# Kernel optimization log

Hardware: AMD Instinct MI355X
Metric: run time of the kernel (lower is better)

## Reference

```python
import jax, jax.numpy as jnp
import numpy as np

L, D, F, H = 4, 1024, 2048, 8
DH = D // H
EPS = 1e-5


def setup_inputs() -> dict:
    key = jax.random.key(0)
    ks = jax.random.split(key, 8)
    B, S = 4, 1024
    sd = 1.0 / np.sqrt(D)
    sf = 1.0 / np.sqrt(F)
    return {
        "X": jax.random.normal(ks[0], (B, S, D), jnp.float32),
        "Wq": jax.random.normal(ks[1], (L, D, D), jnp.float32) * sd,
        "Wk": jax.random.normal(ks[2], (L, D, D), jnp.float32) * sd,
        "Wv": jax.random.normal(ks[3], (L, D, D), jnp.float32) * sd,
        "Wg": jax.random.normal(ks[4], (L, D, D), jnp.float32) * sd,
        "Wo": jax.random.normal(ks[5], (L, D, D), jnp.float32) * sd,
        "W1": jax.random.normal(ks[6], (L, D, F), jnp.float32) * sd,
        "W2": jax.random.normal(ks[7], (L, F, D), jnp.float32) * sf,
        "ln_scale": jnp.ones((D,), jnp.float32),
        "ln_bias": jnp.zeros((D,), jnp.float32),
        "gn_scale": jnp.ones((L, D), jnp.float32),
        "gn_bias": jnp.zeros((L, D), jnp.float32),
    }


def _layer_norm(x, scale, bias):
    mu = x.mean(-1, keepdims=True)
    var = x.var(-1, keepdims=True)
    return (x - mu) * jax.lax.rsqrt(var + EPS) * scale + bias


def _rotate(x, cos, sin):
    # x: (B,S,H,DH); cos/sin: (1,S,1,DH//2); rotary pairs (even, odd)
    x1, x2 = x[..., 0::2], x[..., 1::2]
    r1 = x1 * cos - x2 * sin
    r2 = x1 * sin + x2 * cos
    return jnp.stack([r1, r2], axis=-1).reshape(x.shape)


def _decay_matrix(S):
    # D[h,n,m] = gamma_h^(n-m) for n>=m else 0
    gammas = 1.0 - jnp.exp(jnp.linspace(np.log(1 / 32), np.log(1 / 512), H)).astype(jnp.float32)
    n = jnp.arange(S)
    diff = (n[:, None] - n[None, :]).astype(jnp.float32)
    pw = jnp.exp(jnp.clip(diff, 0.0)[None] * jnp.log(gammas)[:, None, None])
    return jnp.where(diff[None] >= 0, pw, 0.0)  # (H,S,S)


def _retention(x, Wq, Wk, Wv, Wg, Wo, gn_s, gn_b, Dm, cos, sin):
    B, S, _ = x.shape
    Q = (x @ Wq).reshape(B, S, H, DH)
    K = (x @ Wk).reshape(B, S, H, DH)
    V = (x @ Wv).reshape(B, S, H, DH)
    Q = _rotate(Q, cos, sin)
    K = _rotate(K, cos, -sin)  # conjugate phase
    att = jnp.einsum('bnhd,bmhd->bhnm', Q, K) * Dm  # (B,H,S,S)
    Y = jnp.einsum('bhnm,bmhd->bnhd', att, V)
    # group norm: normalize each head's output per token
    mu = Y.mean(-1, keepdims=True)
    var = Y.var(-1, keepdims=True)
    Y = (Y - mu) * jax.lax.rsqrt(var + EPS)
    Y = Y.reshape(B, S, D) * gn_s + gn_b
    G = jax.nn.swish(x @ Wg)
    return (G * Y) @ Wo


def reference(X, Wq, Wk, Wv, Wg, Wo, W1, W2, ln_scale, ln_bias, gn_scale, gn_bias):
    B, S, _ = X.shape
    pos = jnp.arange(S, dtype=jnp.float32)
    inv_freq = 1.0 / (10000.0 ** (jnp.arange(0, DH, 2, dtype=jnp.float32) / DH))
    ang = pos[:, None] * inv_freq[None, :]  # (S, DH//2)
    cos = jnp.cos(ang)[None, :, None, :]
    sin = jnp.sin(ang)[None, :, None, :]
    Dm = _decay_matrix(S)
    for i in range(L):
        Yr = _retention(_layer_norm(X, ln_scale, ln_bias), Wq[i], Wk[i], Wv[i],
                        Wg[i], Wo[i], gn_scale[i], gn_bias[i], Dm, cos, sin) + X
        X = jax.nn.gelu(_layer_norm(Yr, ln_scale, ln_bias) @ W1[i]) @ W2[i] + Yr
    return X
```

## Files before the change

### kernel.cpp

```cpp
#include <hip/hip_runtime.h>
#include <hip/hip_bf16.h>
#include <cmath>

#define LAYERS 4
#define Bb 4
#define Ss 1024
#define Dd 1024
#define Ff 2048
#define Hh 8
#define DHd 128
#define Mm (Bb * Ss)
#define EPSf 1e-5f
#define LDQ 4096

typedef __attribute__((ext_vector_type(8))) short short8v;
typedef __attribute__((ext_vector_type(4))) float f32x4;
typedef __attribute__((ext_vector_type(4))) unsigned int u32x4;

__device__ __forceinline__ float swish_f(float x) { return x / (1.f + expf(-x)); }
__device__ __forceinline__ float gelu_f(float x) {
  return 0.5f * x * (1.f + tanhf(0.7978845608028654f * (x + 0.044715f * x * x * x)));
}
__device__ __forceinline__ unsigned short f2bfu(float f) {
  __hip_bfloat16 h = __float2bfloat16(f);
  return __builtin_bit_cast(unsigned short, h);
}
__device__ __forceinline__ float bfu2f(unsigned short u) {
  unsigned v = ((unsigned)u) << 16;
  return __builtin_bit_cast(float, v);
}
__device__ __forceinline__ void gl_lds16(const void* g, void* l) {
  __builtin_amdgcn_global_load_lds((__attribute__((address_space(1))) void*)g,
                                   (__attribute__((address_space(3))) void*)l, 16, 0, 0);
}
__device__ __forceinline__ f32x4 mfma16(short8v a, short8v b, f32x4 c) {
  return __builtin_amdgcn_mfma_f32_16x16x32_bf16(a, b, c, 0, 0, 0);
}

__global__ __launch_bounds__(256) void ln_bf16_kernel(const float* __restrict__ x,
                                                      short* __restrict__ outb,
                                                      const float* __restrict__ sc,
                                                      const float* __restrict__ bi) {
  const int row = blockIdx.x;
  const int t = threadIdx.x;
  const float4 v = *(const float4*)(x + (size_t)row * Dd + t * 4);
  float s = v.x + v.y + v.z + v.w;
  float s2 = v.x * v.x + v.y * v.y + v.z * v.z + v.w * v.w;
#pragma unroll
  for (int o = 32; o > 0; o >>= 1) { s += __shfl_down(s, o); s2 += __shfl_down(s2, o); }
  __shared__ float ps[4], ps2[4];
  if ((t & 63) == 0) { ps[t >> 6] = s; ps2[t >> 6] = s2; }
  __syncthreads();
  s = ps[0] + ps[1] + ps[2] + ps[3];
  s2 = ps2[0] + ps2[1] + ps2[2] + ps2[3];
  const float mu = s * (1.f / Dd);
  const float var = s2 * (1.f / Dd) - mu * mu;
  const float rstd = rsqrtf(var + EPSf);
  const float4 g = *(const float4*)(sc + t * 4);
  const float4 b = *(const float4*)(bi + t * 4);
  const float o0 = (v.x - mu) * rstd * g.x + b.x;
  const float o1 = (v.y - mu) * rstd * g.y + b.y;
  const float o2 = (v.z - mu) * rstd * g.z + b.z;
  const float o3 = (v.w - mu) * rstd * g.w + b.w;
  unsigned p0 = (unsigned)f2bfu(o0) | ((unsigned)f2bfu(o1) << 16);
  unsigned p1 = (unsigned)f2bfu(o2) | ((unsigned)f2bfu(o3) << 16);
  uint2 pk; pk.x = p0; pk.y = p1;
  *(uint2*)(outb + (size_t)row * Dd + t * 4) = pk;
}

__global__ void rope_table_kernel(float* __restrict__ ct, float* __restrict__ st) {
  const int i = blockIdx.x * 256 + threadIdx.x;
  const int s = i >> 6, f = i & 63;
  const float inv = powf(10000.f, -(float)f / 64.f);
  const float a = (float)s * inv;
  ct[i] = cosf(a);
  st[i] = sinf(a);
}

__global__ __launch_bounds__(256) void wtrans_ln_kernel(
    const float* __restrict__ Wq, const float* __restrict__ Wk,
    const float* __restrict__ Wv, const float* __restrict__ Wg,
    const float* __restrict__ Wo, const float* __restrict__ W1,
    const float* __restrict__ W2,
    short* __restrict__ Wqkvgt, short* __restrict__ Wot,
    short* __restrict__ W1t, short* __restrict__ W2t,
    const float* __restrict__ x, short* __restrict__ outb,
    const float* __restrict__ sc, const float* __restrict__ bi) {
  __shared__ float tile[32][33];
  __shared__ float ps[4], ps2[4];
  const int t = threadIdx.x;
  const int blk = blockIdx.x;
  if (blk >= 9216) {
    const int row = blk - 9216;
    const float4 v = *(const float4*)(x + (size_t)row * Dd + t * 4);
    float s = v.x + v.y + v.z + v.w;
    float s2 = v.x * v.x + v.y * v.y + v.z * v.z + v.w * v.w;
#pragma unroll
    for (int o = 32; o > 0; o >>= 1) { s += __shfl_down(s, o); s2 += __shfl_down(s2, o); }
    if ((t & 63) == 0) { ps[t >> 6] = s; ps2[t >> 6] = s2; }
    __syncthreads();
    s = ps[0] + ps[1] + ps[2] + ps[3];
    s2 = ps2[0] + ps2[1] + ps2[2] + ps2[3];
    const float mu = s * (1.f / Dd);
    const float var = s2 * (1.f / Dd) - mu * mu;
    const float rstd = rsqrtf(var + EPSf);
    const float4 g = *(const float4*)(sc + t * 4);
    const float4 b = *(const float4*)(bi + t * 4);
    const float o0 = (v.x - mu) * rstd * g.x + b.x;
    const float o1 = (v.y - mu) * rstd * g.y + b.y;
    const float o2 = (v.z - mu) * rstd * g.z + b.z;
    const float o3 = (v.w - mu) * rstd * g.w + b.w;
    unsigned p0 = (unsigned)f2bfu(o0) | ((unsigned)f2bfu(o1) << 16);
    unsigned p1 = (unsigned)f2bfu(o2) | ((unsigned)f2bfu(o3) << 16);
    uint2 pk; pk.x = p0; pk.y = p1;
    *(uint2*)(outb + (size_t)row * Dd + t * 4) = pk;
    return;
  }
  const int tc = t & 31, tr8 = t >> 5;
  const float* src; short* dst; int K, N, n0, k0, nl;
  if (blk < 4096) {
    const int bx = blk & 127, ky = blk >> 7;
    n0 = bx * 32; k0 = ky * 32;
    const int which = n0 >> 10;
    src = (which == 0) ? Wq : (which == 1) ? Wk : (which == 2) ? Wv : Wg;
    nl = n0 & 1023; N = 1024; K = 1024; dst = Wqkvgt;
  } else if (blk < 5120) {
    const int b2 = blk - 4096;
    n0 = (b2 & 31) * 32; k0 = (b2 >> 5) * 32; nl = n0;
    src = Wo; N = 1024; K = 1024; dst = Wot;
  } else if (blk < 7168) {
    const int b2 = blk - 5120;
    n0 = (b2 & 63) * 32; k0 = (b2 >> 6) * 32; nl = n0;
    src = W1; N = 2048; K = 1024; dst = W1t;
  } else {
    const int b2 = blk - 7168;
    n0 = (b2 & 31) * 32; k0 = (b2 >> 5) * 32; nl = n0;
    src = W2; N = 1024; K = 2048; dst = W2t;
  }
#pragma unroll
  for (int i = 0; i < 4; ++i) {
    const int r = tr8 + i * 8;
    tile[r][tc] = src[(size_t)(k0 + r) * N + nl + tc];
  }
  __syncthreads();
#pragma unroll
  for (int i = 0; i < 4; ++i) {
    const int r = tr8 + i * 8;
    dst[(size_t)(n0 + r) * K + k0 + tc] = (short)f2bfu(tile[tc][r]);
  }
}

__global__ __launch_bounds__(256) void rvt_kernel(short* __restrict__ QKVGb,
                                                  short* __restrict__ Vt,
                                                  const float* __restrict__ ct,
                                                  const float* __restrict__ st) {
  __shared__ short tile[32][33];
  const int blk = blockIdx.x, t = threadIdx.x;
  if (blk < 8192) {
    const int idx = blk * 256 + t;
    const int f = idx & 63;
    const int h = (idx >> 6) & 7;
    const int r = idx >> 9;
    const int s = r & (Ss - 1);
    const float c = ct[(s << 6) + f], sn = st[(s << 6) + f];
    const size_t qo = (size_t)r * LDQ + h * DHd + 2 * f;
    const unsigned qp = *(const unsigned*)(QKVGb + qo);
    const unsigned kp = *(const unsigned*)(QKVGb + qo + 1024);
    const float qx = bfu2f((unsigned short)(qp & 0xffff)), qy = bfu2f((unsigned short)(qp >> 16));
    const float kx = bfu2f((unsigned short)(kp & 0xffff)), ky = bfu2f((unsigned short)(kp >> 16));
    const unsigned qn = (unsigned)f2bfu(qx * c - qy * sn) |
                        ((unsigned)f2bfu(qx * sn + qy * c) << 16);
    const unsigned kn = (unsigned)f2bfu(kx * c + ky * sn) |
                        ((unsigned)f2bfu(-kx * sn + ky * c) << 16);
    *(unsigned*)(QKVGb + qo) = qn;
    *(unsigned*)(QKVGb + qo + 1024) = kn;
  } else {
    const int vb = blk - 8192;
    const int s0 = (vb & 31) * 32, d0 = ((vb >> 5) & 3) * 32, bh = vb >> 7;
    const int bb = bh >> 3, h = bh & 7;
    const int tc = t & 31, tr8 = t >> 5;
#pragma unroll
    for (int i = 0; i < 4; ++i) {
      const int r = tr8 + i * 8;
      tile[r][tc] = QKVGb[(size_t)(bb * Ss + s0 + r) * LDQ + 2048 + h * DHd + d0 + tc];
    }
    __syncthreads();
#pragma unroll
    for (int i = 0; i < 4; ++i) {
      const int r = tr8 + i * 8;
      Vt[(size_t)(bh * DHd + d0 + r) * Ss + s0 + tc] = tile[tc][r];
    }
  }
}

template <int EPI>
__global__ __launch_bounds__(512, 2) void gemm10(const short* __restrict__ A,
                                                 const short* __restrict__ Bt,
                                                 float* __restrict__ Cf,
                                                 short* __restrict__ Cb,
                                                 const float* __restrict__ Res,
                                                 int N, int K, int ldc) {
  __shared__ __align__(16) short As[2][2][128 * 64];
  __shared__ __align__(16) short Bs[2][2][128 * 64];
  const int t = threadIdx.x;
  const int w = t >> 6, l = t & 63;
  const int lq = l >> 4, lr = l & 15;
  const int wr = w >> 2, wc = w & 3;
  const int bhalf = wc >> 1, brow0 = (wc & 1) * 64;
  const int nwg = gridDim.x * gridDim.y;
  const int bid0 = blockIdx.x + blockIdx.y * gridDim.x;
  const int lgid = (bid0 & 7) * (nwg >> 3) + (bid0 >> 3);
  const int bx = lgid % gridDim.x, by = lgid / gridDim.x;
  const int row0 = by * 256, col0 = bx * 256;
  const int NT = K >> 6;

  f32x4 acc[8][4] = {};
  short8v a[4][2], b[4][2];

  auto stageA = [&](int kt, int hf) {
    const int db = kt & 1;
#pragma unroll
    for (int i = 0; i < 2; ++i) {
      const int c = t + i * 512;
      const int row = c >> 3, slot = c & 7;
      gl_lds16(A + (size_t)(row0 + hf * 128 + row) * K + kt * 64 + ((slot ^ (row & 7)) << 3),
               &As[db][hf][c * 8]);
    }
  };
  auto stageB = [&](int kt, int hf) {
    const int db = kt & 1;
#pragma unroll
    for (int i = 0; i < 2; ++i) {
      const int c = t + i * 512;
      const int row = c >> 3, slot = c & 7;
      gl_lds16(Bt + (size_t)(col0 + hf * 128 + row) * K + kt * 64 + ((slot ^ (row & 7)) << 3),
               &Bs[db][hf][c * 8]);
    }
  };
  auto rdA = [&](int db, int m, int ks) -> short8v {
    const int row = m * 16 + lr;
    return *(const short8v*)&As[db][wr][row * 64 + (((ks << 2) + lq) ^ (row & 7)) * 8];
  };
  auto rdB = [&](int db, int n, int ks) -> short8v {
    const int row = brow0 + n * 16 + lr;
    return *(const short8v*)&Bs[db][bhalf][row * 64 + (((ks << 2) + lq) ^ (row & 7)) * 8];
  };

  stageA(0, 0); stageA(0, 1); stageB(0, 0); stageB(0, 1);
  if (NT > 1) { stageB(1, 0); stageB(1, 1); }
  if (NT > 1) { asm volatile("s_waitcnt vmcnt(4)" ::: "memory"); }
  else        { asm volatile("s_waitcnt vmcnt(0)" ::: "memory"); }
  asm volatile("s_barrier" ::: "memory");

  for (int kt = 0; kt < NT; ++kt) {
    const int db = kt & 1;
#pragma unroll
    for (int m = 0; m < 4; ++m) { a[m][0] = rdA(db, m, 0); a[m][1] = rdA(db, m, 1); }
#pragma unroll
    for (int n = 0; n < 2; ++n) { b[n][0] = rdB(db, n, 0); b[n][1] = rdB(db, n, 1); }
    if (kt + 1 < NT) stageA(kt + 1, 0);
    __builtin_amdgcn_s_setprio(1);
#pragma unroll
    for (int m = 0; m < 4; ++m)
#pragma unroll
      for (int n = 0; n < 2; ++n) {
        acc[m][n] = mfma16(a[m][0], b[n][0], acc[m][n]);
        acc[m][n] = mfma16(a[m][1], b[n][1], acc[m][n]);
      }
    __builtin_amdgcn_s_setprio(0);
    asm volatile("s_barrier" ::: "memory");
#pragma unroll
    for (int n = 2; n < 4; ++n) { b[n][0] = rdB(db, n, 0); b[n][1] = rdB(db, n, 1); }
    if (kt + 1 < NT) stageA(kt + 1, 1);
    __builtin_amdgcn_s_setprio(1);
#pragma unroll
    for (int m = 0; m < 4; ++m)
#pragma unroll
      for (int n = 2; n < 4; ++n) {
        acc[m][n] = mfma16(a[m][0], b[n][0], acc[m][n]);
        acc[m][n] = mfma16(a[m][1], b[n][1], acc[m][n]);
      }
    __builtin_amdgcn_s_setprio(0);
    asm volatile("s_barrier" ::: "memory");
#pragma unroll
    for (int m = 0; m < 4; ++m) { a[m][0] = rdA(db, m + 4, 0); a[m][1] = rdA(db, m + 4, 1); }
    if (kt + 2 < NT) stageB(kt + 2, 0);
    __builtin_amdgcn_s_setprio(1);
#pragma unroll
    for (int m = 0; m < 4; ++m)
#pragma unroll
      for (int n = 0; n < 2; ++n) {
        acc[m + 4][n] = mfma16(a[m][0], b[n][0], acc[m + 4][n]);
        acc[m + 4][n] = mfma16(a[m][1], b[n][1], acc[m + 4][n]);
      }
    __builtin_amdgcn_s_setprio(0);
    asm volatile("s_barrier" ::: "memory");
    if (kt + 2 < NT) stageB(kt + 2, 1);
    __builtin_amdgcn_s_setprio(1);
#pragma unroll
    for (int m = 0; m < 4; ++m)
#pragma unroll
      for (int n = 2; n < 4; ++n) {
        acc[m + 4][n] = mfma16(a[m][0], b[n][0], acc[m + 4][n]);
        acc[m + 4][n] = mfma16(a[m][1], b[n][1], acc[m + 4][n]);
      }
    __builtin_amdgcn_s_setprio(0);
    if (kt + 2 < NT) { asm volatile("s_waitcnt vmcnt(4)" ::: "memory"); }
    else             { asm volatile("s_waitcnt vmcnt(0)" ::: "memory"); }
    asm volatile("s_barrier" ::: "memory");
  }

#pragma unroll
  for (int m = 0; m < 8; ++m) {
#pragma unroll
    for (int n = 0; n < 4; ++n) {
#pragma unroll
      for (int r = 0; r < 4; ++r) {
        const int row = row0 + wr * 128 + m * 16 + lq * 4 + r;
        const int col = col0 + wc * 64 + n * 16 + lr;
        const size_t o = (size_t)row * ldc + col;
        float v = acc[m][n][r];
        if (EPI == 0) Cb[o] = (short)f2bfu(v);
        else if (EPI == 1) Cf[o] = v + Res[o];
        else Cb[o] = (short)f2bfu(gelu_f(v));
      }
    }
  }
}

template <int EPI>
__global__ __launch_bounds__(512) void gemm11(const short* __restrict__ A,
                                              const short* __restrict__ Bt,
                                              float* __restrict__ Cf,
                                              short* __restrict__ Cb,
                                              const float* __restrict__ Res,
                                              int K, int lda, int ldb, int ldc, int nxt) {
  __shared__ __align__(16) short As[3][256 * 64];
  __shared__ __align__(16) short Bs[3][128 * 64];
  const int t = threadIdx.x;
  const int w = t >> 6, l = t & 63;
  const int lq = l >> 4, lr = l & 15;
  const int wr = w >> 2, wc = w & 3;
  const int nwg = gridDim.x;
  const int lgid = (blockIdx.x & 7) * (nwg >> 3) + (blockIdx.x >> 3);
  const int mt = lgid / nxt, nt_ = lgid % nxt;
  const int row0 = mt * 256, col0 = nt_ * 128;
  const int NT = K >> 6;
  f32x4 acc[8][2] = {};
  short8v a[4][2], b[2][2];

  auto stageA = [&](int kt, int hf) {
    const int s = kt % 3;
#pragma unroll
    for (int i = 0; i < 2; ++i) {
      const int c = t + i * 512;
      const int row = c >> 3, slot = c & 7;
      gl_lds16(A + (size_t)(row0 + hf * 128 + row) * lda + kt * 64 + ((slot ^ (row & 7)) << 3),
               &As[s][hf * 8192 + c * 8]);
    }
  };
  auto stageB = [&](int kt) {
    const int s = kt % 3;
#pragma unroll
    for (int i = 0; i < 2; ++i) {
      const int c = t + i * 512;
      const int row = c >> 3, slot = c & 7;
      gl_lds16(Bt + (size_t)(col0 + row) * ldb + kt * 64 + ((slot ^ (row & 7)) << 3),
               &Bs[s][c * 8]);
    }
  };
  auto rdA = [&](int s, int m, int ks) -> short8v {
    const int row = wr * 128 + m * 16 + lr;
    return *(const short8v*)&As[s][row * 64 + (((ks << 2) + lq) ^ (row & 7)) * 8];
  };
  auto rdB = [&](int s, int n, int ks) -> short8v {
    const int row = wc * 32 + n * 16 + lr;
    return *(const short8v*)&Bs[s][row * 64 + (((ks << 2) + lq) ^ (row & 7)) * 8];
  };

  stageA(0, 0); stageA(0, 1); stageB(0);
  stageA(1, 0); stageA(1, 1); stageB(1);
  asm volatile("s_waitcnt vmcnt(6)" ::: "memory");
  asm volatile("s_barrier" ::: "memory");

  for (int kt = 0; kt < NT; ++kt) {
    const int s = kt % 3;
#pragma unroll
    for (int m = 0; m < 4; ++m) { a[m][0] = rdA(s, m, 0); a[m][1] = rdA(s, m, 1); }
#pragma unroll
    for (int n = 0; n < 2; ++n) { b[n][0] = rdB(s, n, 0); b[n][1] = rdB(s, n, 1); }
    if (kt + 2 < NT) stageA(kt + 2, 0);
    __builtin_amdgcn_s_setprio(1);
#pragma unroll
    for (int m = 0; m < 4; ++m)
#pragma unroll
      for (int n = 0; n < 2; ++n) {
        acc[m][n] = mfma16(a[m][0], b[n][0], acc[m][n]);
        acc[m][n] = mfma16(a[m][1], b[n][1], acc[m][n]);
      }
    __builtin_amdgcn_s_setprio(0);
    asm volatile("s_barrier" ::: "memory");
#pragma unroll
    for (int m = 0; m < 4; ++m) { a[m][0] = rdA(s, m + 4, 0); a[m][1] = rdA(s, m + 4, 1); }
    if (kt + 2 < NT) { stageA(kt + 2, 1); stageB(kt + 2); }
    __builtin_amdgcn_s_setprio(1);
#pragma unroll
    for (int m = 0; m < 4; ++m)
#pragma unroll
      for (int n = 0; n < 2; ++n) {
        acc[m + 4][n] = mfma16(a[m][0], b[n][0], acc[m + 4][n]);
        acc[m + 4][n] = mfma16(a[m][1], b[n][1], acc[m + 4][n]);
      }
    __builtin_amdgcn_s_setprio(0);
    if (kt + 2 < NT) { asm volatile("s_waitcnt vmcnt(6)" ::: "memory"); }
    else             { asm volatile("s_waitcnt vmcnt(0)" ::: "memory"); }
    asm volatile("s_barrier" ::: "memory");
  }

#pragma unroll
  for (int m = 0; m < 8; ++m) {
#pragma unroll
    for (int n = 0; n < 2; ++n) {
#pragma unroll
      for (int r = 0; r < 4; ++r) {
        const int row = row0 + wr * 128 + m * 16 + lq * 4 + r;
        const int col = col0 + wc * 32 + n * 16 + lr;
        const size_t o = (size_t)row * ldc + col;
        float v = acc[m][n][r];
        if (EPI == 0) Cb[o] = (short)f2bfu(v);
        else if (EPI == 1) Cf[o] = v + Res[o];
        else Cb[o] = (short)f2bfu(gelu_f(v));
      }
    }
  }
}

template <int EPI>
__global__ __launch_bounds__(512) void gemm12(const short* __restrict__ A,
                                              const short* __restrict__ Bt,
                                              float* __restrict__ Cf,
                                              short* __restrict__ Cb,
                                              const float* __restrict__ Res,
                                              int K, int lda, int ldb, int ldc, int nxt) {
  __shared__ __align__(16) short As[3][128 * 64];
  __shared__ __align__(16) short Bs[3][128 * 64];
  const int t = threadIdx.x;
  const int w = t >> 6, l = t & 63;
  const int lq = l >> 4, lr = l & 15;
  const int wr = w >> 2, wc = w & 3;
  const int nwg = gridDim.x;
  const int lgid = (blockIdx.x & 7) * (nwg >> 3) + (blockIdx.x >> 3);
  const int mt = lgid / nxt, nt_ = lgid % nxt;
  const int row0 = mt * 128, col0 = nt_ * 128;
  const int NT = K >> 6;
  f32x4 acc[4][2] = {};
  short8v a[4][2], b[2][2];

  auto stageA = [&](int kt) {
    const int s = kt % 3;
#pragma unroll
    for (int i = 0; i < 2; ++i) {
      const int c = t + i * 512;
      const int row = c >> 3, slot = c & 7;
      gl_lds16(A + (size_t)(row0 + row) * lda + kt * 64 + ((slot ^ (row & 7)) << 3),
               &As[s][c * 8]);
    }
  };
  auto stageB = [&](int kt) {
    const int s = kt % 3;
#pragma unroll
    for (int i = 0; i < 2; ++i) {
      const int c = t + i * 512;
      const int row = c >> 3, slot = c & 7;
      gl_lds16(Bt + (size_t)(col0 + row) * ldb + kt * 64 + ((slot ^ (row & 7)) << 3),
               &Bs[s][c * 8]);
    }
  };
  auto rdA = [&](int s, int m, int ks) -> short8v {
    const int row = wr * 64 + m * 16 + lr;
    return *(const short8v*)&As[s][row * 64 + (((ks << 2) + lq) ^ (row & 7)) * 8];
  };
  auto rdB = [&](int s, int n, int ks) -> short8v {
    const int row = wc * 32 + n * 16 + lr;
    return *(const short8v*)&Bs[s][row * 64 + (((ks << 2) + lq) ^ (row & 7)) * 8];
  };

  stageA(0); stageB(0);
  stageA(1); stageB(1);
  asm volatile("s_waitcnt vmcnt(4)" ::: "memory");
  asm volatile("s_barrier" ::: "memory");

  for (int kt = 0; kt < NT; ++kt) {
    const int s = kt % 3;
#pragma unroll
    for (int m = 0; m < 4; ++m) { a[m][0] = rdA(s, m, 0); a[m][1] = rdA(s, m, 1); }
#pragma unroll
    for (int n = 0; n < 2; ++n) { b[n][0] = rdB(s, n, 0); b[n][1] = rdB(s, n, 1); }
    if (kt + 2 < NT) stageA(kt + 2);
    __builtin_amdgcn_s_setprio(1);
#pragma unroll
    for (int m = 0; m < 2; ++m)
#pragma unroll
      for (int n = 0; n < 2; ++n) {
        acc[m][n] = mfma16(a[m][0], b[n][0], acc[m][n]);
        acc[m][n] = mfma16(a[m][1], b[n][1], acc[m][n]);
      }
    __builtin_amdgcn_s_setprio(0);
    asm volatile("s_barrier" ::: "memory");
    if (kt + 2 < NT) stageB(kt + 2);
    __builtin_amdgcn_s_setprio(1);
#pragma unroll
    for (int m = 2; m < 4; ++m)
#pragma unroll
      for (int n = 0; n < 2; ++n) {
        acc[m][n] = mfma16(a[m][0], b[n][0], acc[m][n]);
        acc[m][n] = mfma16(a[m][1], b[n][1], acc[m][n]);
      }
    __builtin_amdgcn_s_setprio(0);
    if (kt + 2 < NT) { asm volatile("s_waitcnt vmcnt(4)" ::: "memory"); }
    else             { asm volatile("s_waitcnt vmcnt(0)" ::: "memory"); }
    asm volatile("s_barrier" ::: "memory");
  }

#pragma unroll
  for (int m = 0; m < 4; ++m) {
#pragma unroll
    for (int n = 0; n < 2; ++n) {
#pragma unroll
      for (int r = 0; r < 4; ++r) {
        const int row = row0 + wr * 64 + m * 16 + lq * 4 + r;
        const int col = col0 + wc * 32 + n * 16 + lr;
        const size_t o = (size_t)row * ldc + col;
        float v = acc[m][n][r];
        if (EPI == 0) Cb[o] = (short)f2bfu(v);
        else if (EPI == 1) Cf[o] = v + Res[o];
        else Cb[o] = (short)f2bfu(gelu_f(v));
      }
    }
  }
}

__global__ __launch_bounds__(256) void ret5_kernel(const short* __restrict__ QKVGb,
                                                   const short* __restrict__ Vt,
                                                   short* __restrict__ Gb,
                                                   const float* __restrict__ gs,
                                                   const float* __restrict__ gb) {
  __shared__ __align__(16) short Ks[2][64 * 128];
  __shared__ __align__(16) short Vs[2][128 * 64];
  const int t = threadIdx.x, w = t >> 6, l = t & 63;
  const int lq = l >> 4, lr = l & 15;
  const int u = blockIdx.x;
  const int lgid = (u & 7) * 32 + (u >> 3);
  const int bh = lgid >> 3, pr = lgid & 7;
  const int b = bh >> 3, h = bh & 7;
  const float lstep = (logf(1.f / 512.f) - logf(1.f / 32.f)) * (1.f / 7.f);
  const float gamma = 1.f - expf(logf(1.f / 32.f) + (float)h * lstep);
  const float l2g = logf(gamma) * 1.44269504f;
  const short* Qp = QKVGb;
  const short* Kp = QKVGb + 1024;

  float cmf[4], csr[4];
#pragma unroll
  for (int mf = 0; mf < 4; ++mf) cmf[mf] = exp2f(l2g * (float)(-16 * mf));
#pragma unroll
  for (int r = 0; r < 4; ++r) csr[r] = exp2f(l2g * (float)(63 - 4 * lq - r));
  float gsv[8], gbv[8];
#pragma unroll
  for (int nd = 0; nd < 8; ++nd) {
    gsv[nd] = gs[h * DHd + nd * 16 + lr];
    gbv[nd] = gb[h * DHd + nd * 16 + lr];
  }
  const int sb = ((lq & 1) * 2) * 16 + lr;

  auto stageKV = [&](int m0, int buf) {
#pragma unroll
    for (int i = 0; i < 4; ++i) {
      const int c = (w * 4 + i) * 64 + l;
      const int row = c >> 4, slot = c & 15;
      gl_lds16(Kp + (size_t)(b * Ss + m0 + row) * LDQ + h * DHd + ((slot ^ (row & 7)) * 8),
               &Ks[buf][(w * 4 + i) * 512]);
    }
#pragma unroll
    for (int i = 0; i < 4; ++i) {
      const int c = (w * 4 + i) * 64 + l;
      const int row = c >> 3, slot = c & 7;
      gl_lds16(Vt + (size_t)(bh * DHd + row) * Ss + m0 + ((slot ^ (row & 7)) * 8),
               &Vs[buf][(w * 4 + i) * 512]);
    }
  };

  for (int pass = 0; pass < 2; ++pass) {
    const int qb = pass ? (15 - pr) : pr;
    const int q0 = qb * 64;
    const int nt = qb + 1;
    short8v qf[4];
#pragma unroll
    for (int ks = 0; ks < 4; ++ks)
      qf[ks] = *(const short8v*)(Qp + (size_t)(b * Ss + q0 + w * 16 + lr) * LDQ +
                                 h * DHd + ks * 32 + lq * 8);
    f32x4 yacc[8] = {};
    stageKV(0, 0);
    __syncthreads();
    int cur = 0;
    for (int tt = 0; tt < nt; ++tt) {
      const int m0 = tt * 64;
      if (tt + 1 < nt) stageKV((tt + 1) * 64, cur ^ 1);

      f32x4 st[4] = {};
      __builtin_amdgcn_s_setprio(1);
#pragma unroll
      for (int mf = 0; mf < 4; ++mf) {
        const int row = mf * 16 + lr;
#pragma unroll
        for (int ks = 0; ks < 4; ++ks) {
          short8v kf = *(const short8v*)&Ks[cur][row * 128 + (((4 * ks + lq) ^ (row & 7)) * 8)];
          st[mf] = mfma16(kf, qf[ks], st[mf]);
        }
      }
      __builtin_amdgcn_s_setprio(0);
      const int qg = q0 + w * 16 + lr;
      const float rs = exp2f(l2g * (float)(qg - m0 - 63));
#pragma unroll
      for (int mf = 0; mf < 4; ++mf)
#pragma unroll
        for (int r = 0; r < 4; ++r) {
          const int kvg = m0 + mf * 16 + lq * 4 + r;
          const float wgt = (qg >= kvg) ? rs * cmf[mf] * csr[r] : 0.f;
          st[mf][r] *= wgt;
        }
      unsigned pk[4][2];
#pragma unroll
      for (int mf = 0; mf < 4; ++mf)
#pragma unroll
        for (int p = 0; p < 2; ++p)
          pk[mf][p] = (unsigned)f2bfu(st[mf][2 * p]) |
                      ((unsigned)f2bfu(st[mf][2 * p + 1]) << 16);
      short8v afr[2];
#pragma unroll
      for (int ks2 = 0; ks2 < 2; ++ks2) {
        u32x4 wd;
#pragma unroll
        for (int wj = 0; wj < 4; ++wj) {
          const int src = sb + (wj >> 1) * 16;
          const unsigned v0 = __shfl(pk[2 * ks2 + 0][wj & 1], src);
          const unsigned v1 = __shfl(pk[2 * ks2 + 1][wj & 1], src);
          wd[wj] = (lq >= 2) ? v1 : v0;
        }
        afr[ks2] = __builtin_bit_cast(short8v, wd);
      }
      __builtin_amdgcn_s_setprio(1);
#pragma unroll
      for (int nd = 0; nd < 8; ++nd) {
        const int row = nd * 16 + lr;
#pragma unroll
        for (int ks2 = 0; ks2 < 2; ++ks2) {
          short8v vf = *(const short8v*)&Vs[cur][row * 64 + (((4 * ks2 + lq) ^ (row & 7)) * 8)];
          yacc[nd] = mfma16(afr[ks2], vf, yacc[nd]);
        }
      }
      __builtin_amdgcn_s_setprio(0);
      __syncthreads();
      cur ^= 1;
    }
#pragma unroll
    for (int r = 0; r < 4; ++r) {
      float s1 = 0.f, s2 = 0.f;
#pragma unroll
      for (int nd = 0; nd < 8; ++nd) { const float v = yacc[nd][r]; s1 += v; s2 += v * v; }
#pragma unroll
      for (int msk = 1; msk < 16; msk <<= 1) {
        s1 += __shfl_xor(s1, msk);
        s2 += __shfl_xor(s2, msk);
      }
      const float mu = s1 * (1.f / 128.f);
      const float rstd = rsqrtf(s2 * (1.f / 128.f) - mu * mu + EPSf);
      const int q = q0 + w * 16 + lq * 4 + r;
      const size_t gbase = (size_t)(b * Ss + q) * LDQ + 3072 + h * DHd;
      const size_t obase = (size_t)(b * Ss + q) * Dd + h * DHd;
#pragma unroll
      for (int nd = 0; nd < 8; ++nd) {
        const int d = nd * 16 + lr;
        const float yv = (yacc[nd][r] - mu) * rstd * gsv[nd] + gbv[nd];
        const float gvx = bfu2f((unsigned short)QKVGb[gbase + d]);
        Gb[obase + d] = (short)f2bfu(swish_f(gvx) * yv);
      }
    }
  }
}

extern "C" void kernel_launch(void* const* d_in, const int* in_sizes, int n_in,
                              void* d_out, int out_size, void* d_ws, size_t ws_size,
                              hipStream_t stream) {
  const float* X = (const float*)d_in[0];
  const float* Wq = (const float*)d_in[1];
  const float* Wk = (const float*)d_in[2];
  const float* Wv = (const float*)d_in[3];
  const float* Wg = (const float*)d_in[4];
  const float* Wo = (const float*)d_in[5];
  const float* W1 = (const float*)d_in[6];
  const float* W2 = (const float*)d_in[7];
  const float* lns = (const float*)d_in[8];
  const float* lnb = (const float*)d_in[9];
  const float* gns = (const float*)d_in[10];
  const float* gnb = (const float*)d_in[11];
  float* out = (float*)d_out;

  char* W = (char*)d_ws;
  const size_t MB = 1u << 20;
  float* Abuf  = (float*)(W);
  short* Xnb   = (short*)(W + 16 * MB);
  short* QKVGb = (short*)(W + 24 * MB);
  short* Vtb   = (short*)(W + 88 * MB);
  short* Gb    = (short*)(W + 96 * MB);
  short* Wqkvgt= (short*)(W + 104 * MB);
  short* Wot   = (short*)(W + 112 * MB);
  short* W1t   = (short*)(W + 114 * MB);
  short* W2t   = (short*)(W + 118 * MB);
  float* ct    = (float*)(W + 122 * MB);
  float* st    = ct + Ss * 64;
  short* Hb = QKVGb;

  rope_table_kernel<<<(Ss * 64) / 256, 256, 0, stream>>>(ct, st);

  for (int l = 0; l < LAYERS; ++l) {
    const size_t DD = (size_t)Dd * Dd;
    const float* Acur = (l == 0) ? X : Abuf;
    wtrans_ln_kernel<<<13312, 256, 0, stream>>>(Wq + l * DD, Wk + l * DD, Wv + l * DD,
                                                Wg + l * DD, Wo + l * DD,
                                                W1 + (size_t)l * Dd * Ff,
                                                W2 + (size_t)l * Ff * Dd,
                                                Wqkvgt, Wot, W1t, W2t,
                                                Acur, Xnb, lns, lnb);
    gemm10<0><<<dim3(16, 16), 512, 0, stream>>>(Xnb, Wqkvgt, nullptr, QKVGb,
                                                nullptr, 4096, Dd, LDQ);
    rvt_kernel<<<12288, 256, 0, stream>>>(QKVGb, Vtb, ct, st);
    ret5_kernel<<<256, 256, 0, stream>>>(QKVGb, Vtb, Gb,
                                         gns + (size_t)l * Dd, gnb + (size_t)l * Dd);
    gemm12<1><<<256, 512, 0, stream>>>(Gb, Wot, Abuf, nullptr, Acur,
                                       Dd, Dd, Dd, Dd, 8);
    ln_bf16_kernel<<<Mm, 256, 0, stream>>>(Abuf, Xnb, lns, lnb);
    gemm11<2><<<256, 512, 0, stream>>>(Xnb, W1t, nullptr, Hb, nullptr,
                                       Dd, Dd, Dd, Ff, 16);
    float* dst = (l == LAYERS - 1) ? out : Abuf;
    gemm12<1><<<256, 512, 0, stream>>>(Hb, W2t, dst, nullptr, Abuf,
                                       Ff, Ff, Ff, Dd, 8);
  }
}
```

Before: 701.4 us.

## Fuse V transpose into QKVG GEMM epilogue via LDS staging

The V columns of the fused QKVG projection GEMM are now transposed in shared memory inside the epilogue and written straight to the Vt buffer. This removes the separate transpose half of the rotary/transpose kernel, which becomes a rope-only kernel. The GEMM's shared arrays are merged into one flat buffer so the 256x256 output tile can be staged with an XOR swizzle before the transposed 8-byte stores. V blocks no longer write V into the row-major QKVG buffer, so correctness depends on nothing downstream reading V from there.

```diff
diff --git a/kernel.cpp b/kernel.cpp
--- a/kernel.cpp
+++ b/kernel.cpp
@@ -150,47 +150,26 @@
   }
 }
 
-__global__ __launch_bounds__(256) void rvt_kernel(short* __restrict__ QKVGb,
-                                                  short* __restrict__ Vt,
-                                                  const float* __restrict__ ct,
-                                                  const float* __restrict__ st) {
-  __shared__ short tile[32][33];
-  const int blk = blockIdx.x, t = threadIdx.x;
-  if (blk < 8192) {
-    const int idx = blk * 256 + t;
-    const int f = idx & 63;
-    const int h = (idx >> 6) & 7;
-    const int r = idx >> 9;
-    const int s = r & (Ss - 1);
-    const float c = ct[(s << 6) + f], sn = st[(s << 6) + f];
-    const size_t qo = (size_t)r * LDQ + h * DHd + 2 * f;
-    const unsigned qp = *(const unsigned*)(QKVGb + qo);
-    const unsigned kp = *(const unsigned*)(QKVGb + qo + 1024);
-    const float qx = bfu2f((unsigned short)(qp & 0xffff)), qy = bfu2f((unsigned short)(qp >> 16));
-    const float kx = bfu2f((unsigned short)(kp & 0xffff)), ky = bfu2f((unsigned short)(kp >> 16));
-    const unsigned qn = (unsigned)f2bfu(qx * c - qy * sn) |
-                        ((unsigned)f2bfu(qx * sn + qy * c) << 16);
-    const unsigned kn = (unsigned)f2bfu(kx * c + ky * sn) |
-                        ((unsigned)f2bfu(-kx * sn + ky * c) << 16);
-    *(unsigned*)(QKVGb + qo) = qn;
-    *(unsigned*)(QKVGb + qo + 1024) = kn;
-  } else {
-    const int vb = blk - 8192;
-    const int s0 = (vb & 31) * 32, d0 = ((vb >> 5) & 3) * 32, bh = vb >> 7;
-    const int bb = bh >> 3, h = bh & 7;
-    const int tc = t & 31, tr8 = t >> 5;
-#pragma unroll
-    for (int i = 0; i < 4; ++i) {
-      const int r = tr8 + i * 8;
-      tile[r][tc] = QKVGb[(size_t)(bb * Ss + s0 + r) * LDQ + 2048 + h * DHd + d0 + tc];
-    }
-    __syncthreads();
-#pragma unroll
-    for (int i = 0; i < 4; ++i) {
-      const int r = tr8 + i * 8;
-      Vt[(size_t)(bh * DHd + d0 + r) * Ss + s0 + tc] = tile[tc][r];
-    }
-  }
+__global__ __launch_bounds__(256) void rope_qk_kernel(short* __restrict__ QKVGb,
+                                                      const float* __restrict__ ct,
+                                                      const float* __restrict__ st) {
+  const int idx = blockIdx.x * 256 + threadIdx.x;
+  const int f = idx & 63;
+  const int h = (idx >> 6) & 7;
+  const int r = idx >> 9;
+  const int s = r & (Ss - 1);
+  const float c = ct[(s << 6) + f], sn = st[(s << 6) + f];
+  const size_t qo = (size_t)r * LDQ + h * DHd + 2 * f;
+  const unsigned qp = *(const unsigned*)(QKVGb + qo);
+  const unsigned kp = *(const unsigned*)(QKVGb + qo + 1024);
+  const float qx = bfu2f((unsigned short)(qp & 0xffff)), qy = bfu2f((unsigned short)(qp >> 16));
+  const float kx = bfu2f((unsigned short)(kp & 0xffff)), ky = bfu2f((unsigned short)(kp >> 16));
+  const unsigned qn = (unsigned)f2bfu(qx * c - qy * sn) |
+                      ((unsigned)f2bfu(qx * sn + qy * c) << 16);
+  const unsigned kn = (unsigned)f2bfu(kx * c + ky * sn) |
+                      ((unsigned)f2bfu(-kx * sn + ky * c) << 16);
+  *(unsigned*)(QKVGb + qo) = qn;
+  *(unsigned*)(QKVGb + qo + 1024) = kn;
 }
 
 template <int EPI>
@@ -199,9 +178,9 @@
                                                  float* __restrict__ Cf,
                                                  short* __restrict__ Cb,
                                                  const float* __restrict__ Res,
+                                                 short* __restrict__ Vt,
                                                  int N, int K, int ldc) {
-  __shared__ __align__(16) short As[2][2][128 * 64];
-  __shared__ __align__(16) short Bs[2][2][128 * 64];
+  __shared__ __align__(16) short SM[65536];
   const int t = threadIdx.x;
   const int w = t >> 6, l = t & 63;
   const int lq = l >> 4, lr = l & 15;
@@ -219,31 +198,35 @@
 
   auto stageA = [&](int kt, int hf) {
     const int db = kt & 1;
+    short* dstb = SM + (db * 2 + hf) * 8192;
 #pragma unroll
     for (int i = 0; i < 2; ++i) {
       const int c = t + i * 512;
       const int row = c >> 3, slot = c & 7;
       gl_lds16(A + (size_t)(row0 + hf * 128 + row) * K + kt * 64 + ((slot ^ (row & 7)) << 3),
-               &As[db][hf][c * 8]);
+               dstb + c * 8);
     }
   };
   auto stageB = [&](int kt, int hf) {
     const int db = kt & 1;
+    short* dstb = SM + 32768 + (db * 2 + hf) * 8192;
 #pragma unroll
     for (int i = 0; i < 2; ++i) {
       const int c = t + i * 512;
       const int row = c >> 3, slot = c & 7;
       gl_lds16(Bt + (size_t)(col0 + hf * 128 + row) * K + kt * 64 + ((slot ^ (row & 7)) << 3),
-               &Bs[db][hf][c * 8]);
+               dstb + c * 8);
     }
   };
   auto rdA = [&](int db, int m, int ks) -> short8v {
     const int row = m * 16 + lr;
-    return *(const short8v*)&As[db][wr][row * 64 + (((ks << 2) + lq) ^ (row & 7)) * 8];
+    return *(const short8v*)(SM + (db * 2 + wr) * 8192 + row * 64 +
+                             (((ks << 2) + lq) ^ (row & 7)) * 8);
   };
   auto rdB = [&](int db, int n, int ks) -> short8v {
     const int row = brow0 + n * 16 + lr;
-    return *(const short8v*)&Bs[db][bhalf][row * 64 + (((ks << 2) + lq) ^ (row & 7)) * 8];
+    return *(const short8v*)(SM + 32768 + (db * 2 + bhalf) * 8192 + row * 64 +
+                             (((ks << 2) + lq) ^ (row & 7)) * 8);
   };
 
   stageA(0, 0); stageA(0, 1); stageB(0, 0); stageB(0, 1);
@@ -308,6 +291,46 @@
     if (kt + 2 < NT) { asm volatile("s_waitcnt vmcnt(4)" ::: "memory"); }
     else             { asm volatile("s_waitcnt vmcnt(0)" ::: "memory"); }
     asm volatile("s_barrier" ::: "memory");
+  }
+
+  if (EPI == 0 && col0 >= 2048 && col0 < 3072) {
+#pragma unroll
+    for (int m = 0; m < 8; ++m)
+#pragma unroll
+      for (int n = 0; n < 4; ++n)
+#pragma unroll
+        for (int r = 0; r < 4; ++r) {
+          const int ls = wr * 128 + m * 16 + lq * 4 + r;
+          const int ld = wc * 64 + n * 16 + lr;
+          SM[ld * 256 + ((((ls >> 3) ^ (ld & 31)) << 3) | (ls & 7))] =
+              (short)f2bfu(acc[m][n][r]);
+        }
+    __syncthreads();
+    const int bI = row0 >> 10;
+    const int s0g = row0 & 1023;
+#pragma unroll 4
+    for (int rr = 0; rr < 32; ++rr) {
+      const int dl = w * 32 + rr;
+      const int gcol = (col0 - 2048) + dl;
+      const int hh = gcol >> 7, dh = gcol & 127;
+      unsigned pk0, pk1;
+      {
+        const int s0 = l * 4;
+        const unsigned short e0 =
+            (unsigned short)SM[dl * 256 + ((((s0 + 0) >> 3) ^ (dl & 31)) << 3 | ((s0 + 0) & 7))];
+        const unsigned short e1 =
+            (unsigned short)SM[dl * 256 + ((((s0 + 1) >> 3) ^ (dl & 31)) << 3 | ((s0 + 1) & 7))];
+        const unsigned short e2 =
+            (unsigned short)SM[dl * 256 + ((((s0 + 2) >> 3) ^ (dl & 31)) << 3 | ((s0 + 2) & 7))];
+        const unsigned short e3 =
+            (unsigned short)SM[dl * 256 + ((((s0 + 3) >> 3) ^ (dl & 31)) << 3 | ((s0 + 3) & 7))];
+        pk0 = (unsigned)e0 | ((unsigned)e1 << 16);
+        pk1 = (unsigned)e2 | ((unsigned)e3 << 16);
+      }
+      uint2 pk; pk.x = pk0; pk.y = pk1;
+      *(uint2*)(Vt + ((size_t)((bI * 8 + hh) * 128 + dh)) * Ss + s0g + l * 4) = pk;
+    }
+    return;
   }
 
 #pragma unroll
@@ -732,8 +755,8 @@
                                                 Wqkvgt, Wot, W1t, W2t,
                                                 Acur, Xnb, lns, lnb);
     gemm10<0><<<dim3(16, 16), 512, 0, stream>>>(Xnb, Wqkvgt, nullptr, QKVGb,
-                                                nullptr, 4096, Dd, LDQ);
-    rvt_kernel<<<12288, 256, 0, stream>>>(QKVGb, Vtb, ct, st);
+                                                nullptr, Vtb, 4096, Dd, LDQ);
+    rope_qk_kernel<<<8192, 256, 0, stream>>>(QKVGb, ct, st);
     ret5_kernel<<<256, 256, 0, stream>>>(QKVGb, Vtb, Gb,
                                          gns + (size_t)l * Dd, gnb + (size_t)l * Dd);
     gemm12<1><<<256, 512, 0, stream>>>(Gb, Wot, Abuf, nullptr, Acur,
```

Result: faster. 685.4 us, median of 3 (-2.3%).
